# Performance work log

Measured on AMD Instinct MI355X. Metric: run time of the kernel, lower is better.

The kernel has to match this reference:

```python
import jax, jax.numpy as jnp
import numpy as np

N = 1_000_000          # number of query points
POINT_DIMS = 2         # (x, y) coordinates
NUM_EMB = 6572         # number of video frames
EMB_DIM = 32
HIDDEN = 128


def setup_inputs() -> dict:
    key = jax.random.key(0)
    ks = jax.random.split(key, 10)
    x = jax.random.uniform(ks[0], (N, POINT_DIMS), dtype=jnp.float32)
    # fractional frame index in [0, NUM_EMB - 1)
    embeddings = jax.random.uniform(ks[1], (N,), dtype=jnp.float32) * (NUM_EMB - 1)
    em_table = jax.random.normal(ks[2], (NUM_EMB, EMB_DIM), dtype=jnp.float32) * 0.1
    in0 = POINT_DIMS + EMB_DIM
    W0 = jax.random.normal(ks[3], (in0, HIDDEN), dtype=jnp.float32) / np.sqrt(in0)
    b0 = jax.random.normal(ks[4], (HIDDEN,), dtype=jnp.float32) * 0.01
    W1 = jax.random.normal(ks[5], (HIDDEN, HIDDEN), dtype=jnp.float32) / np.sqrt(HIDDEN)
    b1 = jax.random.normal(ks[6], (HIDDEN,), dtype=jnp.float32) * 0.01
    W2 = jax.random.normal(ks[7], (HIDDEN, 1), dtype=jnp.float32) / np.sqrt(HIDDEN)
    b2 = jax.random.normal(ks[8], (1,), dtype=jnp.float32) * 0.01
    return {"x": x, "embeddings": embeddings, "em_table": em_table,
            "W0": W0, "b0": b0, "W1": W1, "b1": b1, "W2": W2, "b2": b2}


def reference(x, embeddings, em_table, W0, b0, W1, b1, W2, b2):
    num_emb = em_table.shape[0]
    em1 = embeddings.astype(jnp.int32)                       # floor (inputs >= 0)
    em2 = jnp.minimum(em1 + 1, num_emb - 1)                  # clamp(em1+1, max=E-1)
    res = (embeddings - em1.astype(jnp.float32))[:, None]    # [N, 1]
    e1 = em_table[em1]                                       # [N, 32] gather
    e2 = em_table[em2]                                       # [N, 32] gather
    em = e1 + (e2 - e1) * res                                # lerp
    h = jnp.concatenate((x, em), axis=1) @ W0 + b0           # [N, 128]
    h = jnp.clip(h, 0.0, 1.0)
    h = jnp.clip(h @ W1 + b1, 0.0, 1.0)
    out = jax.nn.sigmoid(h @ W2 + b2)                        # [N, 1]
    return out
```

## Files before the change

### kernel.cpp

```cpp
#include <hip/hip_runtime.h>
#include <hip/hip_bf16.h>


using bf16x8 = __attribute__((ext_vector_type(8))) short;
using f32x4  = __attribute__((ext_vector_type(4))) float;

#define NPTS    1000000
#define NUMEMB  6572
#define HID     128
#define M_IT    64
#define A0S     72
#define H0S     136
#define TILES   (NPTS / M_IT)
#define NBLOCKS 768

__device__ __forceinline__ unsigned short bf16r(float f) {
    unsigned u;
    __builtin_memcpy(&u, &f, 4);
    u = (u + 0x7fffu + ((u >> 16) & 1u)) >> 16;
    return (unsigned short)u;
}
__device__ __forceinline__ unsigned pk2(float a, float b) {
    float2 f2; f2.x = a; f2.y = b;
    __hip_bfloat162 h = __float22bfloat162_rn(f2);
    unsigned u;
    __builtin_memcpy(&u, &h, 4);
    return u;
}
__device__ __forceinline__ float clamp01(float x) {
    return __builtin_amdgcn_fmed3f(x, 0.f, 1.f);
}

__global__ __launch_bounds__(256, 3)
void mlp_fused(const float* __restrict__ x,
               const float* __restrict__ emb,
               const float* __restrict__ em_table,
               const float* __restrict__ W0, const float* __restrict__ b0,
               const float* __restrict__ W1, const float* __restrict__ b1,
               const float* __restrict__ W2, const float* __restrict__ b2,
               float* __restrict__ out)
{
    __shared__ __align__(16) unsigned short A0[M_IT * A0S];
    __shared__ __align__(16) unsigned short H0[M_IT * H0S];
    __shared__ __align__(16) float PART[16][M_IT];

    const int tid  = threadIdx.x;
    const int lane = tid & 63;
    const int nq   = tid >> 6;
    const int q    = lane >> 4;
    const int cl   = lane & 15;
    const int p    = tid >> 2;
    const int s    = tid & 3;

    for (int i = tid; i < M_IT * A0S; i += 256) A0[i] = 0;

    const int hcol = nq * 32 + (cl >> 2) * 8 + (cl & 3);
    bf16x8 w0t[2][2];
    for (int hb = 0; hb < 2; ++hb)
        for (int kt = 0; kt < 2; ++kt) {
            const int col = hcol + hb * 4;
            bf16x8 v;
            #pragma unroll
            for (int e = 0; e < 8; ++e) {
                const int k = kt * 32 + q * 8 + e;
                float val = 0.f;
                if (k < 32)       val = W0[(2 + k) * HID + col];
                else if (k == 32) val = W0[0 * HID + col];
                else if (k == 33) val = W0[1 * HID + col];
                v[e] = (short)bf16r(val);
            }
            w0t[hb][kt] = v;
        }

    bf16x8 w1r[2][4];
    for (int hb = 0; hb < 2; ++hb)
        for (int kk = 0; kk < 4; ++kk) {
            const int kt  = (nq + kk) & 3;
            const int col = hcol + hb * 4;
            bf16x8 v;
            #pragma unroll
            for (int e = 0; e < 8; ++e) {
                const int k = kt * 32 + q * 8 + e;
                v[e] = (short)bf16r(W1[k * HID + col]);
            }
            w1r[hb][kk] = v;
        }

    f32x4 b0q[2], b1q[2], w2q[2];
    for (int hb = 0; hb < 2; ++hb)
        for (int r = 0; r < 4; ++r) {
            const int h = nq * 32 + q * 8 + hb * 4 + r;
            b0q[hb][r] = b0[h];
            b1q[hb][r] = b1[h];
            w2q[hb][r] = W2[h];
        }
    const float bias2 = b2[0];

    int t = blockIdx.x;
    float  feA;
    float2 xvA = {0.f, 0.f};
    {
        const int gp = t * M_IT + p;
        feA = emb[gp];
        if (s == 0) xvA = *(const float2*)(x + 2 * gp);
    }

    __syncthreads();

    for (; t < TILES; t += gridDim.x) {
        const int base = t * M_IT;

        {
            const int e1 = (int)feA;
            const int e2 = (e1 + 1 < NUMEMB) ? e1 + 1 : NUMEMB - 1;
            const float r = feA - (float)e1;
            const float4* p1 = (const float4*)(em_table + e1 * 32 + s * 8);
            const float4* p2 = (const float4*)(em_table + e2 * 32 + s * 8);
            const float4 a0v = p1[0], a1v = p1[1];
            const float4 c0v = p2[0], c1v = p2[1];
            uint4 d;
            d.x = pk2(a0v.x + (c0v.x - a0v.x) * r, a0v.y + (c0v.y - a0v.y) * r);
            d.y = pk2(a0v.z + (c0v.z - a0v.z) * r, a0v.w + (c0v.w - a0v.w) * r);
            d.z = pk2(a1v.x + (c1v.x - a1v.x) * r, a1v.y + (c1v.y - a1v.y) * r);
            d.w = pk2(a1v.z + (c1v.z - a1v.z) * r, a1v.w + (c1v.w - a1v.w) * r);
            *(uint4*)&A0[p * A0S + s * 8] = d;
            if (s == 0) *(unsigned*)&A0[p * A0S + 32] = pk2(xvA.x, xvA.y);
        }
        __syncthreads();

        f32x4 acc[4][2];
        #pragma unroll
        for (int pb = 0; pb < 4; ++pb)
            #pragma unroll
            for (int hb = 0; hb < 2; ++hb)
                acc[pb][hb] = b0q[hb];
        #pragma unroll
        for (int pb = 0; pb < 4; ++pb) {
            #pragma unroll
            for (int kt = 0; kt < 2; ++kt) {
                bf16x8 bfrag = *(const bf16x8*)
                    &A0[(pb * 16 + cl) * A0S + kt * 32 + q * 8];
                #pragma unroll
                for (int hb = 0; hb < 2; ++hb)
                    acc[pb][hb] = __builtin_amdgcn_mfma_f32_16x16x32_bf16(
                        w0t[hb][kt], bfrag, acc[pb][hb], 0, 0, 0);
            }
        }

        {
            int t1 = t + gridDim.x; if (t1 >= TILES) t1 = t;
            const int gp = t1 * M_IT + p;
            feA = emb[gp];
            if (s == 0) xvA = *(const float2*)(x + 2 * gp);
        }

        uint4 own[4];
        #pragma unroll
        for (int pb = 0; pb < 4; ++pb) {
            const f32x4 v0 = acc[pb][0], v1 = acc[pb][1];
            uint4 w;
            w.x = pk2(clamp01(v0[0]), clamp01(v0[1]));
            w.y = pk2(clamp01(v0[2]), clamp01(v0[3]));
            w.z = pk2(clamp01(v1[0]), clamp01(v1[1]));
            w.w = pk2(clamp01(v1[2]), clamp01(v1[3]));
            own[pb] = w;
            *(uint4*)&H0[(pb * 16 + cl) * H0S + nq * 32 + q * 8] = w;
        }
        __syncthreads();

        #pragma unroll
        for (int pb = 0; pb < 4; ++pb)
            #pragma unroll
            for (int hb = 0; hb < 2; ++hb)
                acc[pb][hb] = b1q[hb];
        #pragma unroll
        for (int pb = 0; pb < 4; ++pb) {
            bf16x8 bfrag;
            __builtin_memcpy(&bfrag, &own[pb], 16);
            #pragma unroll
            for (int hb = 0; hb < 2; ++hb)
                acc[pb][hb] = __builtin_amdgcn_mfma_f32_16x16x32_bf16(
                    w1r[hb][0], bfrag, acc[pb][hb], 0, 0, 0);
        }
        #pragma unroll
        for (int kk = 1; kk < 4; ++kk) {
            const int kcol = (((nq + kk) & 3) << 5) + q * 8;
            #pragma unroll
            for (int pb = 0; pb < 4; ++pb) {
                bf16x8 bfrag = *(const bf16x8*)
                    &H0[(pb * 16 + cl) * H0S + kcol];
                #pragma unroll
                for (int hb = 0; hb < 2; ++hb)
                    acc[pb][hb] = __builtin_amdgcn_mfma_f32_16x16x32_bf16(
                        w1r[hb][kk], bfrag, acc[pb][hb], 0, 0, 0);
            }
        }

        #pragma unroll
        for (int pb = 0; pb < 4; ++pb) {
            float sum = 0.f;
            #pragma unroll
            for (int hb = 0; hb < 2; ++hb) {
                const f32x4 v = acc[pb][hb];
                sum += clamp01(v[0]) * w2q[hb][0];
                sum += clamp01(v[1]) * w2q[hb][1];
                sum += clamp01(v[2]) * w2q[hb][2];
                sum += clamp01(v[3]) * w2q[hb][3];
            }
            PART[nq * 4 + q][pb * 16 + cl] = sum;
        }
        __syncthreads();

        if (tid < 64) {
            float z = bias2;
            #pragma unroll
            for (int i = 0; i < 16; ++i) z += PART[i][tid];
            out[base + tid] = 1.f / (1.f + __expf(-z));
        }
    }
}

extern "C" void kernel_launch(void* const* d_in, const int* in_sizes, int n_in,
                              void* d_out, int out_size, void* d_ws, size_t ws_size,
                              hipStream_t stream) {
    const float* x   = (const float*)d_in[0];
    const float* emb = (const float*)d_in[1];
    const float* emt = (const float*)d_in[2];
    const float* W0  = (const float*)d_in[3];
    const float* b0  = (const float*)d_in[4];
    const float* W1  = (const float*)d_in[5];
    const float* b1  = (const float*)d_in[6];
    const float* W2  = (const float*)d_in[7];
    const float* b2  = (const float*)d_in[8];
    mlp_fused<<<NBLOCKS, 256, 0, stream>>>(x, emb, emt, W0, b0, W1, b1, W2, b2,
                                           (float*)d_out);
}
```

Baseline: 125.8 us.

## Compute final layer with MFMA, fuse clamp into bf16 pack, double occupancy

The output layer's dot product now runs as an extra MFMA per point block, using a W2 fragment populated only in lane rows with cl==0. Partial sums go into spare padding of the A0 buffer instead of a separate PART array, which cuts LDS use. Clamping is folded into a v_cvt_pk_bf16_f32 clamp instruction, and the biases feed the MFMA accumulators directly. Launch bounds rise to 6 blocks per CU with twice as many blocks, which risks register spills and adds bf16 rounding of the final hidden activations and W2.

```diff
diff --git a/kernel.cpp b/kernel.cpp
--- a/kernel.cpp
+++ b/kernel.cpp
@@ -12,7 +12,7 @@
 #define A0S     72
 #define H0S     136
 #define TILES   (NPTS / M_IT)
-#define NBLOCKS 768
+#define NBLOCKS 1536
 
 __device__ __forceinline__ unsigned short bf16r(float f) {
     unsigned u;
@@ -27,11 +27,13 @@
     __builtin_memcpy(&u, &h, 4);
     return u;
 }
-__device__ __forceinline__ float clamp01(float x) {
-    return __builtin_amdgcn_fmed3f(x, 0.f, 1.f);
-}
-
-__global__ __launch_bounds__(256, 3)
+__device__ __forceinline__ unsigned pk2c(float a, float b) {
+    unsigned r;
+    asm("v_cvt_pk_bf16_f32 %0, %1, %2 clamp" : "=v"(r) : "v"(a), "v"(b));
+    return r;
+}
+
+__global__ __launch_bounds__(256, 6)
 void mlp_fused(const float* __restrict__ x,
                const float* __restrict__ emb,
                const float* __restrict__ em_table,
@@ -42,7 +44,6 @@
 {
     __shared__ __align__(16) unsigned short A0[M_IT * A0S];
     __shared__ __align__(16) unsigned short H0[M_IT * H0S];
-    __shared__ __align__(16) float PART[16][M_IT];
 
     const int tid  = threadIdx.x;
     const int lane = tid & 63;
@@ -86,14 +87,17 @@
             w1r[hb][kk] = v;
         }
 
-    f32x4 b0q[2], b1q[2], w2q[2];
+    f32x4 b0q[2], b1q[2];
     for (int hb = 0; hb < 2; ++hb)
         for (int r = 0; r < 4; ++r) {
             const int h = nq * 32 + q * 8 + hb * 4 + r;
             b0q[hb][r] = b0[h];
             b1q[hb][r] = b1[h];
-            w2q[hb][r] = W2[h];
-        }
+        }
+    bf16x8 w2f;
+    #pragma unroll
+    for (int e = 0; e < 8; ++e)
+        w2f[e] = (cl == 0) ? (short)bf16r(W2[nq * 32 + q * 8 + e]) : (short)0;
     const float bias2 = b2[0];
 
     int t = blockIdx.x;
@@ -130,20 +134,15 @@
 
         f32x4 acc[4][2];
         #pragma unroll
-        for (int pb = 0; pb < 4; ++pb)
-            #pragma unroll
-            for (int hb = 0; hb < 2; ++hb)
-                acc[pb][hb] = b0q[hb];
-        #pragma unroll
-        for (int pb = 0; pb < 4; ++pb) {
-            #pragma unroll
-            for (int kt = 0; kt < 2; ++kt) {
-                bf16x8 bfrag = *(const bf16x8*)
-                    &A0[(pb * 16 + cl) * A0S + kt * 32 + q * 8];
-                #pragma unroll
-                for (int hb = 0; hb < 2; ++hb)
-                    acc[pb][hb] = __builtin_amdgcn_mfma_f32_16x16x32_bf16(
-                        w0t[hb][kt], bfrag, acc[pb][hb], 0, 0, 0);
+        for (int pb = 0; pb < 4; ++pb) {
+            const bf16x8 bf0 = *(const bf16x8*)&A0[(pb * 16 + cl) * A0S + q * 8];
+            const bf16x8 bf1 = *(const bf16x8*)&A0[(pb * 16 + cl) * A0S + 32 + q * 8];
+            #pragma unroll
+            for (int hb = 0; hb < 2; ++hb) {
+                f32x4 a = __builtin_amdgcn_mfma_f32_16x16x32_bf16(
+                    w0t[hb][0], bf0, b0q[hb], 0, 0, 0);
+                acc[pb][hb] = __builtin_amdgcn_mfma_f32_16x16x32_bf16(
+                    w0t[hb][1], bf1, a, 0, 0, 0);
             }
         }
 
@@ -159,28 +158,23 @@
         for (int pb = 0; pb < 4; ++pb) {
             const f32x4 v0 = acc[pb][0], v1 = acc[pb][1];
             uint4 w;
-            w.x = pk2(clamp01(v0[0]), clamp01(v0[1]));
-            w.y = pk2(clamp01(v0[2]), clamp01(v0[3]));
-            w.z = pk2(clamp01(v1[0]), clamp01(v1[1]));
-            w.w = pk2(clamp01(v1[2]), clamp01(v1[3]));
+            w.x = pk2c(v0[0], v0[1]);
+            w.y = pk2c(v0[2], v0[3]);
+            w.z = pk2c(v1[0], v1[1]);
+            w.w = pk2c(v1[2], v1[3]);
             own[pb] = w;
             *(uint4*)&H0[(pb * 16 + cl) * H0S + nq * 32 + q * 8] = w;
         }
         __syncthreads();
 
         #pragma unroll
-        for (int pb = 0; pb < 4; ++pb)
-            #pragma unroll
-            for (int hb = 0; hb < 2; ++hb)
-                acc[pb][hb] = b1q[hb];
-        #pragma unroll
         for (int pb = 0; pb < 4; ++pb) {
             bf16x8 bfrag;
             __builtin_memcpy(&bfrag, &own[pb], 16);
             #pragma unroll
             for (int hb = 0; hb < 2; ++hb)
                 acc[pb][hb] = __builtin_amdgcn_mfma_f32_16x16x32_bf16(
-                    w1r[hb][0], bfrag, acc[pb][hb], 0, 0, 0);
+                    w1r[hb][0], bfrag, b1q[hb], 0, 0, 0);
         }
         #pragma unroll
         for (int kk = 1; kk < 4; ++kk) {
@@ -196,26 +190,28 @@
             }
         }
 
-        #pragma unroll
-        for (int pb = 0; pb < 4; ++pb) {
-            float sum = 0.f;
-            #pragma unroll
-            for (int hb = 0; hb < 2; ++hb) {
-                const f32x4 v = acc[pb][hb];
-                sum += clamp01(v[0]) * w2q[hb][0];
-                sum += clamp01(v[1]) * w2q[hb][1];
-                sum += clamp01(v[2]) * w2q[hb][2];
-                sum += clamp01(v[3]) * w2q[hb][3];
-            }
-            PART[nq * 4 + q][pb * 16 + cl] = sum;
+        const f32x4 zero = {0.f, 0.f, 0.f, 0.f};
+        #pragma unroll
+        for (int pb = 0; pb < 4; ++pb) {
+            const f32x4 v0 = acc[pb][0], v1 = acc[pb][1];
+            uint4 w;
+            w.x = pk2c(v0[0], v0[1]);
+            w.y = pk2c(v0[2], v0[3]);
+            w.z = pk2c(v1[0], v1[1]);
+            w.w = pk2c(v1[2], v1[3]);
+            bf16x8 hf;
+            __builtin_memcpy(&hf, &w, 16);
+            const f32x4 z4 = __builtin_amdgcn_mfma_f32_16x16x32_bf16(
+                w2f, hf, zero, 0, 0, 0);
+            if (q == 0)
+                *(float*)((char*)A0 + (pb * 16 + cl) * 144 + 128 + nq * 4) = z4[0];
         }
         __syncthreads();
 
         if (tid < 64) {
-            float z = bias2;
-            #pragma unroll
-            for (int i = 0; i < 16; ++i) z += PART[i][tid];
-            out[base + tid] = 1.f / (1.f + __expf(-z));
+            const float4 pv = *(const float4*)((const char*)A0 + tid * 144 + 128);
+            const float zz = bias2 + pv.x + pv.y + pv.z + pv.w;
+            out[base + tid] = __builtin_amdgcn_rcpf(1.f + __expf(-zz));
         }
     }
 }
```

After: 257.3 us. +104.5%, slower.
